# Kernel optimization log

Measured on AMD Instinct MI355X. Metric: run time of the kernel, lower is better.

## Reference

```python
import jax, jax.numpy as jnp
import numpy as np

WS = 7          # window size
NH = 12         # num heads
DIM = 384
HD = DIM // NH  # head dim = 32
EPS = 1e-5


def _ln(x, g, b):
    m = x.mean(-1, keepdims=True)
    v = ((x - m) ** 2).mean(-1, keepdims=True)
    return (x - m) / jnp.sqrt(v + EPS) * g + b


def _rel_index():
    # exact replica of WindowAttention.__init__ relative_position_index
    coords = np.stack(np.meshgrid(np.arange(WS), np.arange(WS), indexing='ij'))  # (2,ws,ws)
    flat = coords.reshape(2, -1)                                                 # (2,49)
    rel = flat[:, :, None] - flat[:, None, :]                                    # (2,49,49)
    rel = rel.transpose(1, 2, 0).astype(np.int32)
    rel[:, :, 0] += WS - 1
    rel[:, :, 1] += WS - 1
    rel[:, :, 0] *= 2 * WS - 1
    return jnp.asarray(rel.sum(-1))  # (49,49), values in [0, 169)


def setup_inputs() -> dict:
    key = jax.random.key(0)
    ks = jax.random.split(key, 16)
    B, H, W = 16, 56, 56
    L = H * W
    hidden = int(DIM * 4.0)
    p = lambda k, shp: (jax.random.normal(k, shp, jnp.float32) * 0.02)
    return {
        'x': jax.random.normal(ks[0], (B, L, DIM), jnp.float32),
        'kv': jax.random.normal(ks[1], (2, B, NH, WS * WS, HD), jnp.float32),
        'rel_index': _rel_index(),
        'H': H, 'W': W,
        'g1': jnp.ones((DIM,), jnp.float32), 'b1': jnp.zeros((DIM,), jnp.float32),
        'Wqkv': p(ks[2], (DIM, 3 * DIM)), 'bqkv': jnp.zeros((3 * DIM,), jnp.float32),
        'bias_table': p(ks[3], ((2 * WS - 1) ** 2, NH)),
        'Wproj': p(ks[4], (DIM, DIM)), 'bproj': jnp.zeros((DIM,), jnp.float32),
        'g2': jnp.ones((DIM,), jnp.float32), 'b2': jnp.zeros((DIM,), jnp.float32),
        'Wfc1': p(ks[5], (DIM, hidden)), 'bfc1': jnp.zeros((hidden,), jnp.float32),
        'Wfc2': p(ks[6], (hidden, DIM)), 'bfc2': jnp.zeros((DIM,), jnp.float32),
    }


def reference(x, kv, rel_index, H, W, g1, b1, Wqkv, bqkv, bias_table, Wproj, bproj,
              g2, b2, Wfc1, bfc1, Wfc2, bfc2):
    B, L, C = x.shape
    scale = HD ** -0.5
    nWh, nWw = H // WS, W // WS  # H,W divisible by WS -> pad is a no-op; shift_size=0 -> no roll/mask

    h = _ln(x, g1, b1).reshape(B, H, W, C)
    # window_partition -> (B*nW, N, C), N = WS*WS
    hw = h.reshape(B, nWh, WS, nWw, WS, C).transpose(0, 1, 3, 2, 4, 5).reshape(-1, WS * WS, C)
    B_, N, _ = hw.shape

    qkv = (hw @ Wqkv + bqkv).reshape(B_, N, 3, NH, HD).transpose(2, 0, 3, 1, 4)  # (3,B_,nh,N,hd)
    q = qkv[0] * scale
    k, v = kv[0], kv[1]                     # (B, nh, num_kv, hd)
    reps = B_ // k.shape[0]
    k = jnp.repeat(k, reps, axis=0)         # repeat_interleave: each image's windows share its kv
    v = jnp.repeat(v, reps, axis=0)

    attn = jnp.einsum('bhqd,bhkd->bhqk', q, k)                      # (B_,nh,N,N)
    bias = bias_table[rel_index.reshape(-1)].reshape(N, N, NH).transpose(2, 0, 1)
    attn = jax.nn.softmax(attn + bias[None], axis=-1)
    o = jnp.einsum('bhqk,bhkd->bhqd', attn, v)                      # (B_,nh,N,hd)
    o = o.transpose(0, 2, 1, 3).reshape(B_, N, C) @ Wproj + bproj

    # window_reverse -> (B, L, C)
    o = o.reshape(B, nWh, nWw, WS, WS, C).transpose(0, 1, 3, 2, 4, 5).reshape(B, L, C)
    x = x + o
    x = x + (jax.nn.gelu(_ln(x, g2, b2) @ Wfc1 + bfc1, approximate=False) @ Wfc2 + bfc2)
    return x
```

## Files before the change

kernel.cpp:

```cpp
#include <hip/hip_runtime.h>

typedef __attribute__((ext_vector_type(8))) short short8;
typedef __attribute__((ext_vector_type(4))) float floatx4;
typedef unsigned int u32;

#define DIM 384
#define NHEAD 12
#define HDIM 32

__device__ __forceinline__ float bf2f(unsigned int u) {
    union { unsigned int i; float f; } x; x.i = (u & 0xffffu) << 16; return x.f;
}
__device__ __forceinline__ unsigned short f2bf(float f) {
    union { float f; unsigned int i; } x; x.f = f;
    return (unsigned short)((x.i + 0x7fffu + ((x.i >> 16) & 1u)) >> 16);
}

__device__ __forceinline__ int nat2win(int r) {
    int b = r / 3136; int l = r - b * 3136;
    int hh = l / 56, wc = l - hh * 56;
    int wh = hh / 7, nr = hh - wh * 7;
    int ww = wc / 7, nc = wc - ww * 7;
    return ((b << 6) + wh * 8 + ww) * 49 + nr * 7 + nc;
}
__device__ __forceinline__ int win2nat(int r) {
    int w = r / 49; int n = r - w * 49;
    int b = w >> 6; int wi = w & 63;
    int wh = wi >> 3, ww = wi & 7;
    int hh = wh * 7 + n / 7, wc = ww * 7 + n % 7;
    return b * 3136 + hh * 56 + wc;
}

#define GLOAD_LDS16(g, l) \
    __builtin_amdgcn_global_load_lds((const __attribute__((address_space(1))) u32*)(g), \
                                     (__attribute__((address_space(3))) u32*)(l), 16, 0, 0)

__global__ void transpose_kernel(const float* __restrict__ src,
                                 unsigned short* __restrict__ dst,
                                 int K, int N, int ld) {
    int i = blockIdx.x * blockDim.x + threadIdx.x;
    if (i >= K * N) return;
    int n = i / K, k = i - n * K;
    dst[i] = f2bf(src[(size_t)k * ld + n]);
}

__global__ void bias_expand_kernel(const int* __restrict__ rel_index,
                                   const float* __restrict__ bias_table,
                                   float* __restrict__ biasx) {
    int i = blockIdx.x * blockDim.x + threadIdx.x;
    if (i >= NHEAD * 49 * 49) return;
    int h = i / 2401, r = i - h * 2401;
    biasx[i] = bias_table[rel_index[r] * NHEAD + h];
}

__global__ __launch_bounds__(64) void ln_kernel(const float* __restrict__ x,
                                                const float* __restrict__ g,
                                                const float* __restrict__ b,
                                                unsigned short* __restrict__ out,
                                                int windowed) {
    int r = blockIdx.x;
    int lane = threadIdx.x;
    const float* row = x + (size_t)r * DIM;
    float v[6];
    float s = 0.f, ss = 0.f;
#pragma unroll
    for (int j = 0; j < 3; j++) {
        int c = lane + j * 64;
        float2 f = *(const float2*)(row + 2 * c);
        v[2 * j] = f.x; v[2 * j + 1] = f.y;
        s += f.x + f.y; ss += f.x * f.x + f.y * f.y;
    }
#pragma unroll
    for (int m = 1; m < 64; m <<= 1) {
        s += __shfl_xor(s, m);
        ss += __shfl_xor(ss, m);
    }
    float mean = s * (1.f / DIM);
    float var = ss * (1.f / DIM) - mean * mean;
    float rstd = rsqrtf(var + 1e-5f);
    int orow = windowed ? nat2win(r) : r;
    unsigned short* op = out + (size_t)orow * DIM;
#pragma unroll
    for (int j = 0; j < 3; j++) {
        int c = lane + j * 64;
        float2 gg = *(const float2*)(g + 2 * c);
        float2 bb = *(const float2*)(b + 2 * c);
        float o0 = (v[2 * j] - mean) * rstd * gg.x + bb.x;
        float o1 = (v[2 * j + 1] - mean) * rstd * gg.y + bb.y;
        unsigned int w = ((unsigned int)f2bf(o1) << 16) | f2bf(o0);
        *(unsigned int*)(op + 2 * c) = w;
    }
}

__global__ __launch_bounds__(256) void attn_kernel(const unsigned short* __restrict__ q,
                                                   const float* __restrict__ kv,
                                                   const float* __restrict__ biasx,
                                                   unsigned short* __restrict__ o) {
    __shared__ alignas(16) unsigned short Ks[64 * 40];
    __shared__ alignas(16) unsigned short Vt[32 * 72];
    __shared__ float Bi[49 * 52];
    __shared__ alignas(16) unsigned short Ps[4][16 * 72];

    int blk = blockIdx.x;
    int b = blk / 48; int rem = blk - b * 48;
    int h = rem >> 2; int g = rem & 3;
    size_t row_base = (size_t)(b * 64 + g * 16) * 49;

    int t = threadIdx.x;
    int lane = t & 63;
    int wv = t >> 6;
    int lr = lane & 15;
    int lg = lane >> 4;

    const float* kptr = kv + (size_t)(b * NHEAD + h) * 1568;
    for (int idx = t; idx < 392; idx += 256) {
        int row = idx >> 3, seg = idx & 7;
        float4 f = *(const float4*)(kptr + row * 32 + seg * 4);
        ushort4 h4; h4.x = f2bf(f.x); h4.y = f2bf(f.y); h4.z = f2bf(f.z); h4.w = f2bf(f.w);
        *(ushort4*)&Ks[row * 40 + seg * 4] = h4;
    }
    const float* vptr = kv + (size_t)(192 + b * NHEAD + h) * 1568;
    for (int idx = t; idx < 784; idx += 256) {
        int m = idx >> 4, dp = idx & 15;
        float2 f = *(const float2*)(vptr + m * 32 + dp * 2);
        Vt[(2 * dp) * 72 + m]     = f2bf(f.x);
        Vt[(2 * dp + 1) * 72 + m] = f2bf(f.y);
    }
    for (int idx = t; idx < 32 * 23; idx += 256) {
        int d = idx / 23, m = 49 + idx - d * 23;
        Vt[d * 72 + m] = 0;
    }
    const float* bh = biasx + h * 2401;
    for (int idx = t; idx < 2401; idx += 256) {
        int qr = idx / 49, k = idx - qr * 49;
        Bi[qr * 52 + k] = bh[idx];
    }
    __syncthreads();

    short8 bfr[4], vbf[2][2];
#pragma unroll
    for (int ni = 0; ni < 4; ni++)
        bfr[ni] = *(const short8*)&Ks[(ni * 16 + lr) * 40 + lg * 8];
#pragma unroll
    for (int ni = 0; ni < 2; ni++)
#pragma unroll
        for (int ks = 0; ks < 2; ks++)
            vbf[ni][ks] = *(const short8*)&Vt[(ni * 16 + lr) * 72 + ks * 32 + lg * 8];

    const unsigned short* qb = q + row_base * DIM + h * 32 + lg * 8;
    unsigned short* ob = o + row_base * DIM + h * 32;

    short8 af = *(const short8*)(qb + (size_t)(wv * 16 + lr) * DIM);
    for (int tm = wv; tm < 49; tm += 4) {
        short8 af_next;
        if (tm + 4 < 49) af_next = *(const short8*)(qb + (size_t)((tm + 4) * 16 + lr) * DIM);

        floatx4 sfrag[4];
#pragma unroll
        for (int ni = 0; ni < 4; ni++)
            sfrag[ni] = __builtin_amdgcn_mfma_f32_16x16x32_bf16(af, bfr[ni], (floatx4)0.f, 0, 0, 0);

#pragma unroll
        for (int reg = 0; reg < 4; reg++) {
            int r_loc = tm * 16 + lg * 4 + reg;
            int qr = r_loc % 49;
            float mx = -1e30f;
#pragma unroll
            for (int ni = 0; ni < 4; ni++) {
                int k = ni * 16 + lr;
                float s = sfrag[ni][reg];
                if (k < 49) s += Bi[qr * 52 + k];
                else s = -1e30f;
                sfrag[ni][reg] = s;
                mx = fmaxf(mx, s);
            }
#pragma unroll
            for (int j = 1; j < 16; j <<= 1) mx = fmaxf(mx, __shfl_xor(mx, j));
            float sum = 0.f;
#pragma unroll
            for (int ni = 0; ni < 4; ni++) {
                float e = __expf(sfrag[ni][reg] - mx);
                sfrag[ni][reg] = e;
                sum += e;
            }
#pragma unroll
            for (int j = 1; j < 16; j <<= 1) sum += __shfl_xor(sum, j);
            float inv = 1.f / sum;
#pragma unroll
            for (int ni = 0; ni < 4; ni++)
                Ps[wv][(lg * 4 + reg) * 72 + ni * 16 + lr] = f2bf(sfrag[ni][reg] * inv);
        }
        floatx4 ofrag[2] = {(floatx4)0.f, (floatx4)0.f};
#pragma unroll
        for (int ks = 0; ks < 2; ks++) {
            short8 paf = *(const short8*)&Ps[wv][lr * 72 + ks * 32 + lg * 8];
#pragma unroll
            for (int ni = 0; ni < 2; ni++)
                ofrag[ni] = __builtin_amdgcn_mfma_f32_16x16x32_bf16(paf, vbf[ni][ks], ofrag[ni], 0, 0, 0);
        }
#pragma unroll
        for (int reg = 0; reg < 4; reg++) {
            size_t rg = (size_t)(tm * 16 + lg * 4 + reg) * DIM;
#pragma unroll
            for (int ni = 0; ni < 2; ni++)
                ob[rg + ni * 16 + lr] = f2bf(ofrag[ni][reg]);
        }
        af = af_next;
    }
}

template <int DO_GELU, int DO_REMAP, int OUT_BF16>
__global__ __launch_bounds__(256) void gemm_kernel(const unsigned short* __restrict__ A,
                                                   const unsigned short* __restrict__ Bt,
                                                   const float* __restrict__ bias,
                                                   const float* __restrict__ res,
                                                   void* __restrict__ outv,
                                                   int M, int N, int K, float scale) {
    __shared__ alignas(16) unsigned short As[2][128 * 64];
    __shared__ alignas(16) unsigned short Bs[2][128 * 64];
    int m0 = blockIdx.y * 128;
    int n0 = blockIdx.x * 128;
    int t = threadIdx.x;
    int lane = t & 63;
    int wv = t >> 6;
    int wm = (wv >> 1) * 64, wn = (wv & 1) * 64;
    int lr = lane & 15;
    int lq = lane >> 4;

    int rowB = t >> 3;
    int colOff = (((t & 7) ^ ((t >> 3) & 7)) << 3);
    int sw0 = ((lq ^ (lr & 7)) << 3);
    int sw1 = (((4 + lq) ^ (lr & 7)) << 3);

    floatx4 acc[4][4];
#pragma unroll
    for (int i = 0; i < 4; i++)
#pragma unroll
        for (int j = 0; j < 4; j++) acc[i][j] = (floatx4)0.f;

    auto stage = [&](int buf, int kk) {
#pragma unroll
        for (int i = 0; i < 4; i++) {
            int row = i * 32 + rowB;
            GLOAD_LDS16(A + (size_t)(m0 + row) * K + kk + colOff, &As[buf][(i * 256 + t) * 8]);
            GLOAD_LDS16(Bt + (size_t)(n0 + row) * K + kk + colOff, &Bs[buf][(i * 256 + t) * 8]);
        }
    };

    const int nk = K >> 6;
    stage(0, 0);
    stage(1, 64);

    for (int kt = 0; kt < nk; ++kt) {
        int cur = kt & 1;
        if (kt + 1 < nk) asm volatile("s_waitcnt vmcnt(8)" ::: "memory");
        else             asm volatile("s_waitcnt vmcnt(0)" ::: "memory");
        __builtin_amdgcn_s_barrier();
        asm volatile("" ::: "memory");
#pragma unroll
        for (int ksub = 0; ksub < 2; ksub++) {
            int sw = ksub ? sw1 : sw0;
            short8 af[4], bfr[4];
#pragma unroll
            for (int i = 0; i < 4; i++) {
                af[i] = *(const short8*)(&As[cur][(wm + i * 16 + lr) * 64 + sw]);
                bfr[i] = *(const short8*)(&Bs[cur][(wn + i * 16 + lr) * 64 + sw]);
            }
#pragma unroll
            for (int i = 0; i < 4; i++)
#pragma unroll
                for (int j = 0; j < 4; j++)
                    acc[i][j] = __builtin_amdgcn_mfma_f32_16x16x32_bf16(af[i], bfr[j], acc[i][j], 0, 0, 0);
        }
        __builtin_amdgcn_s_barrier();
        asm volatile("" ::: "memory");
        if (kt + 2 < nk) stage(cur, (kt + 2) << 6);
    }

#pragma unroll
    for (int j = 0; j < 4; j++) {
        int gcol = n0 + wn + j * 16 + lr;
        float bv = bias[gcol];
#pragma unroll
        for (int i = 0; i < 4; i++) {
#pragma unroll
            for (int r = 0; r < 4; r++) {
                int grow = m0 + wm + i * 16 + lq * 4 + r;
                float val = acc[i][j][r] + bv;
                if (DO_GELU) val = 0.5f * val * (1.f + erff(val * 0.70710678118654752f));
                val *= scale;
                int orow = DO_REMAP ? win2nat(grow) : grow;
                size_t idx = (size_t)orow * N + gcol;
                if (res) val += res[idx];
                if (OUT_BF16) ((unsigned short*)outv)[idx] = f2bf(val);
                else          ((float*)outv)[idx] = val;
            }
        }
    }
}

extern "C" void kernel_launch(void* const* d_in, const int* in_sizes, int n_in,
                              void* d_out, int out_size, void* d_ws, size_t ws_size,
                              hipStream_t stream) {
    const float* x          = (const float*)d_in[0];
    const float* kv         = (const float*)d_in[1];
    const int*   rel_index  = (const int*)d_in[2];
    const float* g1         = (const float*)d_in[5];
    const float* b1         = (const float*)d_in[6];
    const float* Wqkv       = (const float*)d_in[7];
    const float* bqkv       = (const float*)d_in[8];
    const float* bias_table = (const float*)d_in[9];
    const float* Wproj      = (const float*)d_in[10];
    const float* bproj      = (const float*)d_in[11];
    const float* g2         = (const float*)d_in[12];
    const float* b2         = (const float*)d_in[13];
    const float* Wfc1       = (const float*)d_in[14];
    const float* bfc1       = (const float*)d_in[15];
    const float* Wfc2       = (const float*)d_in[16];
    const float* bfc2       = (const float*)d_in[17];
    float* out = (float*)d_out;

    char* ws = (char*)d_ws;
    unsigned short* wq_t   = (unsigned short*)(ws);
    unsigned short* wp_t   = (unsigned short*)(ws + 294912);
    unsigned short* wfc1_t = (unsigned short*)(ws + 589824);
    unsigned short* wfc2_t = (unsigned short*)(ws + 1769472);
    float*          biasx  = (float*)(ws + 2949120);
    unsigned short* bufA   = (unsigned short*)(ws + 3080192);
    unsigned short* bufB   = (unsigned short*)(ws + 3080192 + 38535168);

    const int M = 50176;
    const float scale = 0.17677669529663687f;
    const int full_mlp = (ws_size >= (size_t)3080192 + 38535168 + 154140672);

    transpose_kernel<<<(384 * 384 + 255) / 256, 256, 0, stream>>>(Wqkv, wq_t, 384, 384, 1152);
    transpose_kernel<<<(384 * 384 + 255) / 256, 256, 0, stream>>>(Wproj, wp_t, 384, 384, 384);
    transpose_kernel<<<(384 * 1536 + 255) / 256, 256, 0, stream>>>(Wfc1, wfc1_t, 384, 1536, 1536);
    transpose_kernel<<<(1536 * 384 + 255) / 256, 256, 0, stream>>>(Wfc2, wfc2_t, 1536, 384, 384);
    bias_expand_kernel<<<(NHEAD * 2401 + 255) / 256, 256, 0, stream>>>(rel_index, bias_table, biasx);

    ln_kernel<<<M, 64, 0, stream>>>(x, g1, b1, bufA, 1);
    gemm_kernel<0, 0, 1><<<dim3(3, 392), 256, 0, stream>>>(bufA, wq_t, bqkv, nullptr, bufB,
                                                           M, 384, 384, scale);
    attn_kernel<<<16 * NHEAD * 4, 256, 0, stream>>>(bufB, kv, biasx, bufA);
    gemm_kernel<0, 1, 0><<<dim3(3, 392), 256, 0, stream>>>(bufA, wp_t, bproj, x, d_out,
                                                           M, 384, 384, 1.f);
    ln_kernel<<<M, 64, 0, stream>>>(out, g2, b2, bufA, 0);

    if (full_mlp) {
        gemm_kernel<1, 0, 1><<<dim3(12, 392), 256, 0, stream>>>(bufA, wfc1_t, bfc1,
                                                                nullptr, bufB, M, 1536, 384, 1.f);
        gemm_kernel<0, 0, 0><<<dim3(3, 392), 256, 0, stream>>>(bufB, wfc2_t, bfc2,
                                                               out, out, M, 384, 1536, 1.f);
    } else {
        for (int c = 0; c < 4; c++) {
            size_t ro = (size_t)c * 12544;
            gemm_kernel<1, 0, 1><<<dim3(12, 98), 256, 0, stream>>>(bufA + ro * 384, wfc1_t, bfc1,
                                                                   nullptr, bufB, 12544, 1536, 384, 1.f);
            gemm_kernel<0, 0, 0><<<dim3(3, 98), 256, 0, stream>>>(bufB, wfc2_t, bfc2,
                                                                  out + ro * 384, out + ro * 384,
                                                                  12544, 384, 1536, 1.f);
        }
    }
}
```

Baseline: 678.2 us.

## Triple-buffer A tiles, use one barrier per k-step, and remap blocks per XCD

```diff
diff --git a/kernel.cpp b/kernel.cpp
--- a/kernel.cpp
+++ b/kernel.cpp
@@ -216,10 +216,17 @@
                                                    const float* __restrict__ res,
                                                    void* __restrict__ outv,
                                                    int M, int N, int K, float scale) {
-    __shared__ alignas(16) unsigned short As[2][128 * 64];
+    __shared__ alignas(16) unsigned short As[3][128 * 64];
     __shared__ alignas(16) unsigned short Bs[2][128 * 64];
-    int m0 = blockIdx.y * 128;
-    int n0 = blockIdx.x * 128;
+
+    int nwg = gridDim.x * gridDim.y;
+    int lid = blockIdx.y * gridDim.x + blockIdx.x;
+    int q8 = nwg >> 3, r8 = nwg & 7;
+    int xcd = lid & 7, pos = lid >> 3;
+    int nlid = (xcd < r8 ? xcd * (q8 + 1) : r8 * (q8 + 1) + (xcd - r8) * q8) + pos;
+    int m0 = (nlid / gridDim.x) * 128;
+    int n0 = (nlid % gridDim.x) * 128;
+
     int t = threadIdx.x;
     int lane = t & 63;
     int wv = t >> 6;
@@ -238,33 +245,45 @@
 #pragma unroll
         for (int j = 0; j < 4; j++) acc[i][j] = (floatx4)0.f;
 
-    auto stage = [&](int buf, int kk) {
-#pragma unroll
-        for (int i = 0; i < 4; i++) {
-            int row = i * 32 + rowB;
-            GLOAD_LDS16(A + (size_t)(m0 + row) * K + kk + colOff, &As[buf][(i * 256 + t) * 8]);
-            GLOAD_LDS16(Bt + (size_t)(n0 + row) * K + kk + colOff, &Bs[buf][(i * 256 + t) * 8]);
-        }
+    const unsigned short* Abase = A + (size_t)(m0 + rowB) * K + colOff;
+    const unsigned short* Bbase = Bt + (size_t)(n0 + rowB) * K + colOff;
+    size_t rstep = (size_t)32 * K;
+
+    auto stageA = [&](int buf, int kk) {
+#pragma unroll
+        for (int i = 0; i < 4; i++)
+            GLOAD_LDS16(Abase + (size_t)i * rstep + kk, &As[buf][(i * 256 + t) * 8]);
     };
+    auto stageB = [&](int buf, int kk) {
+#pragma unroll
+        for (int i = 0; i < 4; i++)
+            GLOAD_LDS16(Bbase + (size_t)i * rstep + kk, &Bs[buf][(i * 256 + t) * 8]);
+    };
 
     const int nk = K >> 6;
-    stage(0, 0);
-    stage(1, 64);
+
+    stageB(0, 0);
+    stageA(0, 0);
+    stageA(1, 64);
 
     for (int kt = 0; kt < nk; ++kt) {
-        int cur = kt & 1;
-        if (kt + 1 < nk) asm volatile("s_waitcnt vmcnt(8)" ::: "memory");
+        int ab = kt % 3;
+        int bb = kt & 1;
+        if (kt + 1 < nk) asm volatile("s_waitcnt vmcnt(4)" ::: "memory");
         else             asm volatile("s_waitcnt vmcnt(0)" ::: "memory");
         __builtin_amdgcn_s_barrier();
         asm volatile("" ::: "memory");
+        if (kt + 1 < nk) stageB(bb ^ 1, (kt + 1) << 6);
+        if (kt + 2 < nk) stageA((kt + 2) % 3, (kt + 2) << 6);
+        __builtin_amdgcn_s_setprio(1);
 #pragma unroll
         for (int ksub = 0; ksub < 2; ksub++) {
             int sw = ksub ? sw1 : sw0;
             short8 af[4], bfr[4];
 #pragma unroll
             for (int i = 0; i < 4; i++) {
-                af[i] = *(const short8*)(&As[cur][(wm + i * 16 + lr) * 64 + sw]);
-                bfr[i] = *(const short8*)(&Bs[cur][(wn + i * 16 + lr) * 64 + sw]);
+                af[i] = *(const short8*)(&As[ab][(wm + i * 16 + lr) * 64 + sw]);
+                bfr[i] = *(const short8*)(&Bs[bb][(wn + i * 16 + lr) * 64 + sw]);
             }
 #pragma unroll
             for (int i = 0; i < 4; i++)
@@ -272,9 +291,7 @@
                 for (int j = 0; j < 4; j++)
                     acc[i][j] = __builtin_amdgcn_mfma_f32_16x16x32_bf16(af[i], bfr[j], acc[i][j], 0, 0, 0);
         }
-        __builtin_amdgcn_s_barrier();
-        asm volatile("" ::: "memory");
-        if (kt + 2 < nk) stage(cur, (kt + 2) << 6);
+        __builtin_amdgcn_s_setprio(0);
     }
 
 #pragma unroll
```

New measurement: 653.3 us. -3.7%, faster.
